# Kernel tuning notes

Measured on AMD Instinct MI355X. Metric: run time of the kernel, lower is better.

## Reference

```python
import jax, jax.numpy as jnp
import numpy as np

N = 4096          # batch of candidate observations
D = 1024          # embedding dim
N_CLASSES = 100
GTG_MAX_ITER = 30 # gtg_tol=0.0 -> while loop always runs max_iter steps
PERC_LABELED = 0.5
EPS = 1e-8        # matches the +1e-08 in sum_X_A_X


def setup_inputs() -> dict:
    key = jax.random.key(0)
    k1, k2 = jax.random.split(key)
    embedding = jax.random.normal(k1, (N, D), dtype=jnp.float32)
    labels = jax.random.randint(k2, (N,), 0, N_CLASSES, dtype=jnp.int32)
    return {"embedding": embedding, "labels": labels}


def _cos_affinity(E):
    # F.normalize(E, dim=-1) with eps=1e-12, then relu(En @ En.T), diag := 1
    En = E / jnp.maximum(jnp.linalg.norm(E, axis=-1, keepdims=True), 1e-12)
    A = jax.nn.relu(En @ En.T)                      # [N, N]
    n = A.shape[0]
    idx = jnp.arange(n)
    A = A.at[idx, idx].set(1.0)
    return A, En


def reference(embedding, labels):
    n = embedding.shape[0]

    # ---- get_A_rbfk (A_function='cos_sim', rbf_aff=True) ----
    A, En = _cos_affinity(embedding)
    # 7th neighbor by descending cosine similarity (column index 6)
    idx7 = jnp.argsort(-A, axis=1)[:, 6]            # [N]
    # sigma_i = relu(cos(x_i, seventh_i)) -- the [0,1] entry of the 2x2 cos-sim matrix
    sigmas = jax.nn.relu(jnp.sum(En * En[idx7], axis=-1))  # [N]
    A = jnp.exp(-(A ** 2) / (sigmas[:, None] * sigmas[None, :]))

    # ---- threshold (strategy='mean', cos_sim branch) ----
    A = jnp.where(A < jnp.mean(A), 0.0, A)

    # ---- get_X: first n_lab indices labeled (one-hot), rest uniform 1/C ----
    n_lab = int(n * PERC_LABELED)
    labeled = jnp.arange(n) < n_lab                 # [N] bool
    one_hot = jax.nn.one_hot(labels, N_CLASSES, dtype=jnp.float32)
    X0 = jnp.where(labeled[:, None], one_hot, jnp.float32(1.0 / N_CLASSES))

    # ---- graph transduction game: X <- (X + X*(A@X)) / rowsum ----
    def step(X, _):
        mm_A_X = A @ X                              # [N, C]
        mult = X + X * mm_A_X
        Xn = mult / (jnp.sum(mult, axis=1, keepdims=True) + EPS)
        ent = -jnp.sum(Xn * jnp.log(Xn + EPS), axis=1)  # per-row entropy history
        return Xn, ent

    Xf, _ent_hist = jax.lax.scan(step, X0, None, length=GTG_MAX_ITER)
    return Xf
```

## Files before the change

### kernel.cpp

```cpp
#include <hip/hip_runtime.h>
#include <math.h>

typedef unsigned short ushortT;
typedef __attribute__((ext_vector_type(8))) short short8;
typedef __attribute__((ext_vector_type(4))) float f32x4;

#define NN 4096
#define DD 1024
#define NC 100
#define CP 128
#define NLAB 2048
#define NITER 30

__device__ __forceinline__ ushortT bf16rn(float x) {
  unsigned u = __float_as_uint(x);
  unsigned r = (u + 0x7fffu + ((u >> 16) & 1u)) >> 16;
  return (ushortT)r;
}
__device__ __forceinline__ float bf2f(ushortT h) {
  return __uint_as_float(((unsigned)h) << 16);
}
__device__ __forceinline__ void gload16(const void* g, void* l) {
  __builtin_amdgcn_global_load_lds((const __attribute__((address_space(1))) char*)g,
                                   (__attribute__((address_space(3))) char*)l, 16, 0, 0);
}

__global__ __launch_bounds__(256) void k_normalize(const float* __restrict__ E,
                                                   ushortT* __restrict__ Enh) {
  int row = blockIdx.x, t = threadIdx.x;
  const float4* e4 = (const float4*)(E + (size_t)row * DD);
  float4 v = e4[t];
  float ss = v.x * v.x + v.y * v.y + v.z * v.z + v.w * v.w;
  __shared__ float red[4];
  int lane = t & 63, w = t >> 6;
#pragma unroll
  for (int off = 32; off; off >>= 1) ss += __shfl_xor(ss, off);
  if (lane == 0) red[w] = ss;
  __syncthreads();
  float tot = red[0] + red[1] + red[2] + red[3];
  float d = fmaxf(sqrtf(tot), 1e-12f);
  ushort4 hv;
  hv.x = bf16rn(v.x / d); hv.y = bf16rn(v.y / d);
  hv.z = bf16rn(v.z / d); hv.w = bf16rn(v.w / d);
  ((ushort4*)Enh)[(size_t)row * 256 + t] = hv;
}

__global__ __launch_bounds__(256, 4) void k_syrk_mfma(const ushortT* __restrict__ Enh,
                                                      ushortT* __restrict__ A) {
  int xg = (int)blockIdx.x & 7;
  int j = (int)blockIdx.x >> 3;
  int bi = -1, bj = 0;
#pragma unroll
  for (int p = 0; p < 4; ++p) {
    int bic = xg + (p << 3);
    int c = 32 - bic;
    if (bi < 0) {
      if (j < c) { bi = bic; bj = bic + j; } else j -= c;
    }
  }
  if (bi < 0) return;
  __shared__ ushortT lds[18432];
  int t = threadIdx.x;
  int l = t & 63, w = t >> 6;
  int i0 = bi << 7, j0 = bj << 7;
  int wr = w >> 1, wc = w & 1;
  f32x4 zz = {0.f, 0.f, 0.f, 0.f};
  f32x4 acc[4][4];
#pragma unroll
  for (int m = 0; m < 4; ++m)
#pragma unroll
    for (int n = 0; n < 4; ++n) acc[m][n] = zz;
  int arow_l = l & 15, kslot = l >> 4;

  for (int s = 0; s < 16; ++s) {
    int kk0 = s << 6;
#pragma unroll
    for (int q = 0; q < 4; ++q) {
      int n = (q << 8) + t;
      int r = n >> 3, p = n & 7;
      int col = (p ^ (r & 7)) << 3;
      gload16(Enh + (size_t)(i0 + r) * DD + kk0 + col, &lds[n << 3]);
      gload16(Enh + (size_t)(j0 + r) * DD + kk0 + col, &lds[8192 + (n << 3)]);
    }
    __syncthreads();
#pragma unroll
    for (int kk = 0; kk < 2; ++kk) {
      int g = (kk << 2) + kslot;
      short8 av[4], bv[4];
#pragma unroll
      for (int m = 0; m < 4; ++m) {
        int r = (wr << 6) + (m << 4) + arow_l;
        av[m] = *(const short8*)&lds[(r << 6) + ((g ^ (r & 7)) << 3)];
      }
#pragma unroll
      for (int n = 0; n < 4; ++n) {
        int r = (wc << 6) + (n << 4) + arow_l;
        bv[n] = *(const short8*)&lds[8192 + (r << 6) + ((g ^ (r & 7)) << 3)];
      }
#pragma unroll
      for (int m = 0; m < 4; ++m)
#pragma unroll
        for (int n = 0; n < 4; ++n)
          acc[m][n] = __builtin_amdgcn_mfma_f32_16x16x32_bf16(av[m], bv[n], acc[m][n], 0, 0, 0);
    }
    __syncthreads();
  }
  int rbase = (l >> 4) << 2;
#pragma unroll
  for (int m = 0; m < 4; ++m) {
#pragma unroll
    for (int n = 0; n < 4; ++n) {
#pragma unroll
      for (int r = 0; r < 4; ++r) {
        int gi = i0 + (wr << 6) + (m << 4) + rbase + r;
        int gj = j0 + (wc << 6) + (n << 4) + (l & 15);
        float v = fmaxf(acc[m][n][r], 0.0f);
        if (gi == gj) v = 1.0f;
        A[(size_t)gi * NN + gj] = bf16rn(v);
      }
    }
  }
  if (bi != bj) {
    float* T = (float*)&lds[0];
#pragma unroll
    for (int c2 = 0; c2 < 2; ++c2) {
      __syncthreads();
      if (wr == c2) {
#pragma unroll
        for (int m = 0; m < 4; ++m)
#pragma unroll
          for (int n = 0; n < 4; ++n)
#pragma unroll
            for (int r = 0; r < 4; ++r)
              T[(((wc << 6) + (n << 4) + (l & 15)) * 68) + (m << 4) + rbase + r] =
                  fmaxf(acc[m][n][r], 0.0f);
      }
      __syncthreads();
      int lj = t >> 1, cg = (t & 1) << 5;
#pragma unroll
      for (int q = 0; q < 4; ++q) {
        float4 a0 = *(const float4*)&T[lj * 68 + cg + (q << 3)];
        float4 a1 = *(const float4*)&T[lj * 68 + cg + (q << 3) + 4];
        short8 o;
        o[0] = (short)bf16rn(a0.x); o[1] = (short)bf16rn(a0.y);
        o[2] = (short)bf16rn(a0.z); o[3] = (short)bf16rn(a0.w);
        o[4] = (short)bf16rn(a1.x); o[5] = (short)bf16rn(a1.y);
        o[6] = (short)bf16rn(a1.z); o[7] = (short)bf16rn(a1.w);
        *(short8*)&A[(size_t)(j0 + lj) * NN + i0 + (c2 << 6) + cg + (q << 3)] = o;
      }
    }
  }
}

__device__ __forceinline__ void ins7(float (&tv)[7], float v) {
  if (v > tv[6]) {
#pragma unroll
    for (int s = 0; s < 7; s++) {
      if (v > tv[s]) { float tmp = tv[s]; tv[s] = v; v = tmp; }
    }
  }
}
__global__ __launch_bounds__(256) void k_top7(const ushortT* __restrict__ A,
                                              float* __restrict__ sig) {
  int w = threadIdx.x >> 6, lane = threadIdx.x & 63;
  int row = (blockIdx.x << 2) + w;
  const ushortT* a = A + (size_t)row * NN;
  float tv[7];
#pragma unroll
  for (int i = 0; i < 7; i++) tv[i] = -1.0f;
#pragma unroll
  for (int k = 0; k < 8; k++) {
    short8 v = *(const short8*)(a + (k << 9) + (lane << 3));
#pragma unroll
    for (int jj = 0; jj < 8; jj++) ins7(tv, bf2f((ushortT)v[jj]));
  }
  int head = 0;
  float seventh = 0.0f;
  for (int r = 0; r < 7; r++) {
    float h = (head < 7) ? tv[head] : -1.0f;
    float m = h;
#pragma unroll
    for (int off = 32; off; off >>= 1) m = fmaxf(m, __shfl_xor(m, off));
    unsigned long long ball = __ballot(h == m);
    if (lane == (__ffsll(ball) - 1)) head++;
    seventh = m;
  }
  if (lane == 0) sig[row] = seventh;
}

__global__ __launch_bounds__(256) void k_transform(const ushortT* __restrict__ A,
                                                   const float* __restrict__ sig,
                                                   double* __restrict__ parts) {
  int row = blockIdx.x;
  float si = sig[row];
  const ushortT* a = A + (size_t)row * NN;
  int t = threadIdx.x;
  double local = 0.0;
#pragma unroll
  for (int k = 0; k < 2; k++) {
    int idx = (k << 11) + (t << 3);
    short8 v = *(const short8*)(a + idx);
#pragma unroll
    for (int q = 0; q < 2; ++q) {
      float4 sg = *(const float4*)&sig[idx + (q << 2)];
      float s0 = bf2f((ushortT)v[(q << 2) + 0]);
      float s1 = bf2f((ushortT)v[(q << 2) + 1]);
      float s2 = bf2f((ushortT)v[(q << 2) + 2]);
      float s3 = bf2f((ushortT)v[(q << 2) + 3]);
      local += (double)expf(-(s0 * s0) / (si * sg.x)) +
               (double)expf(-(s1 * s1) / (si * sg.y)) +
               (double)expf(-(s2 * s2) / (si * sg.z)) +
               (double)expf(-(s3 * s3) / (si * sg.w));
    }
  }
  __shared__ double dred[4];
  int lane = t & 63, wv = t >> 6;
#pragma unroll
  for (int off = 32; off; off >>= 1) local += __shfl_xor(local, off);
  if (lane == 0) dred[wv] = local;
  __syncthreads();
  if (t == 0) parts[row] = dred[0] + dred[1] + dred[2] + dred[3];
}

__global__ __launch_bounds__(256) void k_mean(const double* __restrict__ parts,
                                              float* __restrict__ meanb) {
  int t = threadIdx.x;
  double local = 0.0;
#pragma unroll
  for (int k = 0; k < NN / 256; k++) local += parts[(k << 8) + t];
  __shared__ double dred[4];
  int lane = t & 63, wv = t >> 6;
#pragma unroll
  for (int off = 32; off; off >>= 1) local += __shfl_xor(local, off);
  if (lane == 0) dred[wv] = local;
  __syncthreads();
  if (t == 0) meanb[0] = (float)((dred[0] + dred[1] + dred[2] + dred[3]) / ((double)NN * (double)NN));
}

__global__ __launch_bounds__(256) void k_thresh_pack(const ushortT* __restrict__ A,
                                                     const float* __restrict__ sig,
                                                     const float* __restrict__ meanb,
                                                     ushortT* __restrict__ ApL,
                                                     ushortT* __restrict__ ApU) {
  float m = meanb[0];
  int i8 = ((int)blockIdx.x << 8) + threadIdx.x;
  int row2 = i8 >> 9;
  int col8 = (i8 & 511) << 3;
  int grow = NLAB + row2;
  float si = sig[grow];
  short8 v = *(const short8*)&A[(size_t)grow * NN + col8];
  short8 o;
#pragma unroll
  for (int q = 0; q < 2; ++q) {
    float4 sg = *(const float4*)&sig[col8 + (q << 2)];
    float s0 = bf2f((ushortT)v[(q << 2) + 0]);
    float s1 = bf2f((ushortT)v[(q << 2) + 1]);
    float s2 = bf2f((ushortT)v[(q << 2) + 2]);
    float s3 = bf2f((ushortT)v[(q << 2) + 3]);
    float c0 = expf(-(s0 * s0) / (si * sg.x));
    float c1 = expf(-(s1 * s1) / (si * sg.y));
    float c2 = expf(-(s2 * s2) / (si * sg.z));
    float c3 = expf(-(s3 * s3) / (si * sg.w));
    o[(q << 2) + 0] = (short)((c0 < m) ? 0 : bf16rn(c0));
    o[(q << 2) + 1] = (short)((c1 < m) ? 0 : bf16rn(c1));
    o[(q << 2) + 2] = (short)((c2 < m) ? 0 : bf16rn(c2));
    o[(q << 2) + 3] = (short)((c3 < m) ? 0 : bf16rn(c3));
  }
  int half = col8 >> 11;
  int cc = col8 & 2047;
  int rt = row2 >> 4, arow = row2 & 15;
  int kc = cc >> 5, khi = (cc >> 3) & 3;
  ushortT* dst = half ? ApU : ApL;
  *(short8*)&dst[((size_t)((rt << 6) + kc) << 9) + (khi << 7) + (arow << 3)] = o;
}

__global__ __launch_bounds__(256) void k_xlabp(const int* __restrict__ labels,
                                               ushortT* __restrict__ Xlabp) {
  int idx = ((int)blockIdx.x << 8) + threadIdx.x;
  int c = idx >> 11, j = idx & 2047;
  int kc = j >> 5, khi = (j >> 3) & 3, k0 = j & 7;
  int cf = c >> 4, slot = c & 15;
  Xlabp[((size_t)(((kc << 3) + cf) << 2) + khi) * 128 + (slot << 3) + k0] =
      (labels[j] == c) ? (ushortT)0x3F80 : (ushortT)0;
}

__global__ __launch_bounds__(64) void k_xinit(float* __restrict__ Xf,
                                              ushortT* __restrict__ Xp) {
  int rt = blockIdx.x, l = threadIdx.x;
  int col = l & 15, rg4 = l >> 4;
  int kc = rt >> 1;
  int kk = ((rt & 1) << 4) + (rg4 << 2);
  int khi = kk >> 3, k0 = kk & 7;
#pragma unroll
  for (int cf = 0; cf < 8; ++cf) {
    int cls = (cf << 4) + col;
    float v = (cls < NC) ? 0.01f : 0.0f;
    ((f32x4*)Xf)[(size_t)((rt << 3) + cf) * 64 + l] = (f32x4){v, v, v, v};
    ushortT h = bf16rn(v);
    ushort4 hv = {h, h, h, h};
    *(ushort4*)&Xp[((size_t)(((kc << 3) + cf) << 2) + khi) * 128 + (col << 3) + k0] = hv;
  }
}

__global__ __launch_bounds__(256) void k_gP(const ushortT* __restrict__ Ap,
                                            const ushortT* __restrict__ Xp,
                                            float* __restrict__ Pp) {
  int t = threadIdx.x, l = t & 63, w = t >> 6;
  int bid = (int)blockIdx.x;
  int rt = ((bid & 7) << 4) + ((bid >> 3) & 15);
  int s = bid >> 7;
  int kc0 = (s << 4) + (w << 2);
  const ushortT* ab = Ap + ((size_t)rt << 15) + ((size_t)kc0 << 9) + (l << 3);
  const ushortT* xb = Xp + ((size_t)kc0 << 12) + (l << 3);
  short8 av[4];
#pragma unroll
  for (int i = 0; i < 4; ++i) av[i] = *(const short8*)(ab + ((size_t)i << 9));
  f32x4 acc[8];
#pragma unroll
  for (int cf = 0; cf < 8; ++cf) {
    acc[cf] = (f32x4){0.f, 0.f, 0.f, 0.f};
#pragma unroll
    for (int i = 0; i < 4; ++i) {
      short8 bv = *(const short8*)(xb + ((size_t)i << 12) + (cf << 9));
      acc[cf] = __builtin_amdgcn_mfma_f32_16x16x32_bf16(av[i], bv, acc[cf], 0, 0, 0);
    }
  }
  __shared__ float red[4][8][64][4];
#pragma unroll
  for (int cf = 0; cf < 8; ++cf) *(f32x4*)&red[w][cf][l][0] = acc[cf];
  __syncthreads();
  if (w < 2) {
#pragma unroll
    for (int q = 0; q < 4; ++q) {
      int cf = (w << 2) + q;
      f32x4 sum = *(const f32x4*)&red[0][cf][l][0];
#pragma unroll
      for (int wp = 1; wp < 4; ++wp) {
        f32x4 p = *(const f32x4*)&red[wp][cf][l][0];
        sum[0] += p[0]; sum[1] += p[1]; sum[2] += p[2]; sum[3] += p[3];
      }
      ((f32x4*)Pp)[((size_t)(((s << 7) + rt) << 3) + cf) * 64 + l] = sum;
    }
  }
}

__global__ __launch_bounds__(64) void k_updY(const float* __restrict__ Pp,
                                             float* __restrict__ YlabF) {
  int rt = blockIdx.x, l = threadIdx.x;
#pragma unroll
  for (int cf = 0; cf < 8; ++cf) {
    f32x4 acc = (f32x4){0.f, 0.f, 0.f, 0.f};
#pragma unroll
    for (int s = 0; s < 4; ++s) {
      f32x4 p = ((const f32x4*)Pp)[((size_t)(((s << 7) + rt) << 3) + cf) * 64 + l];
      acc[0] += p[0]; acc[1] += p[1]; acc[2] += p[2]; acc[3] += p[3];
    }
    ((f32x4*)YlabF)[(size_t)((rt << 3) + cf) * 64 + l] = acc;
  }
}

__global__ __launch_bounds__(256) void k_it2(
    const ushortT* __restrict__ Ap, const ushortT* __restrict__ Xp,
    const float* __restrict__ YlabF, const float* __restrict__ XfPrev,
    float* __restrict__ XfOut, ushortT* __restrict__ XpOut,
    float* __restrict__ sums2, int* __restrict__ cnt2) {
  __shared__ float red[4][4][64][4];
  __shared__ float sums_l[4][16];
  __shared__ float totl[16];
  int t = threadIdx.x, l = t & 63, w = t >> 6;
  int bid = (int)blockIdx.x;
  int rt = ((bid & 7) << 4) + ((bid >> 3) & 15);
  int half = bid >> 7;
  int cf = (half << 2) + w;

  const ushortT* ab = Ap + ((size_t)rt << 15) + ((size_t)(w << 4) << 9) + (l << 3);
  const ushortT* xb = Xp + ((size_t)(w << 4) << 12) + ((size_t)(half << 2) << 9) + (l << 3);
  f32x4 acc[4];
#pragma unroll
  for (int cc = 0; cc < 4; ++cc) acc[cc] = (f32x4){0.f, 0.f, 0.f, 0.f};
#pragma unroll
  for (int i = 0; i < 16; ++i) {
    short8 av = *(const short8*)(ab + ((size_t)i << 9));
#pragma unroll
    for (int cc = 0; cc < 4; ++cc) {
      short8 bv = *(const short8*)(xb + ((size_t)i << 12) + (cc << 9));
      acc[cc] = __builtin_amdgcn_mfma_f32_16x16x32_bf16(av, bv, acc[cc], 0, 0, 0);
    }
  }
#pragma unroll
  for (int cc = 0; cc < 4; ++cc) *(f32x4*)&red[w][cc][l][0] = acc[cc];
  __syncthreads();
  f32x4 mm = (f32x4){0.f, 0.f, 0.f, 0.f};
#pragma unroll
  for (int wp = 0; wp < 4; ++wp) {
    f32x4 p = *(const f32x4*)&red[wp][w][l][0];
    mm[0] += p[0]; mm[1] += p[1]; mm[2] += p[2]; mm[3] += p[3];
  }
  size_t fo = (size_t)((rt << 3) + cf) * 64 + l;
  f32x4 yl = ((const f32x4*)YlabF)[fo];
  f32x4 xv = ((const f32x4*)XfPrev)[fo];
  f32x4 mult, rs;
#pragma unroll
  for (int r = 0; r < 4; ++r) {
    mult[r] = fmaf(xv[r], mm[r] + yl[r], xv[r]);
    rs[r] = mult[r];
  }
#pragma unroll
  for (int msk = 1; msk < 16; msk <<= 1) {
#pragma unroll
    for (int r = 0; r < 4; ++r) rs[r] += __shfl_xor(rs[r], msk);
  }
  int rg4 = l >> 4, col16 = l & 15;
  if (col16 == 0) {
#pragma unroll
    for (int r = 0; r < 4; ++r) sums_l[w][(rg4 << 2) + r] = rs[r];
  }
  __syncthreads();
  if (w == 0 && l < 16) {
    float hs = sums_l[0][l] + sums_l[1][l] + sums_l[2][l] + sums_l[3][l];
    atomicAdd(&sums2[(rt << 4) + l], hs);
  }
  if (t == 0) {
    asm volatile("s_waitcnt vmcnt(0)" ::: "memory");
    atomicAdd(&cnt2[rt], 1);
    while (atomicAdd(&cnt2[rt], 0) < 2) __builtin_amdgcn_s_sleep(2);
  }
  __syncthreads();
  if (w == 0 && l < 16) totl[l] = atomicAdd(&sums2[(rt << 4) + l], 0.0f) + 1e-8f;
  __syncthreads();
  f32x4 ov;
#pragma unroll
  for (int r = 0; r < 4; ++r) ov[r] = mult[r] / totl[(rg4 << 2) + r];
  ((f32x4*)XfOut)[fo] = ov;
  int kcp = rt >> 1;
  int rem = ((rt & 1) << 4) + (rg4 << 2);
  int khi = rem >> 3, k0 = rem & 7;
  ushort4 xo;
  xo.x = bf16rn(ov[0]); xo.y = bf16rn(ov[1]);
  xo.z = bf16rn(ov[2]); xo.w = bf16rn(ov[3]);
  *(ushort4*)&XpOut[((size_t)(((kcp << 3) + cf) << 2) + khi) * 128 + (col16 << 3) + k0] = xo;
}

__global__ __launch_bounds__(256) void k_output(const float* __restrict__ Xf,
                                                const int* __restrict__ labels,
                                                float* __restrict__ out) {
  int idx = ((int)blockIdx.x << 8) + threadIdx.x;
  int i = idx / NC, c = idx - i * NC;
  float v;
  if (i < NLAB) {
    v = (labels[i] == c) ? 1.0f : 0.0f;
  } else {
    int row = i - NLAB;
    int rt = row >> 4, r = row & 15;
    int rg4 = r >> 2, reg = r & 3;
    int cf = c >> 4, col = c & 15;
    v = Xf[((size_t)(((rt << 3) + cf) << 6) + (rg4 << 4) + col) * 4 + reg];
  }
  out[idx] = v;
}

extern "C" void kernel_launch(void* const* d_in, const int* in_sizes, int n_in,
                              void* d_out, int out_size, void* d_ws, size_t ws_size,
                              hipStream_t stream) {
  const float* E = (const float*)d_in[0];
  const int* labels = (const int*)d_in[1];
  float* out = (float*)d_out;
  char* ws = (char*)d_ws;
  const size_t MB = 1024 * 1024;

  ushortT* A = (ushortT*)ws;
  ushortT* Enh = (ushortT*)(ws + 32 * MB);
  ushortT* ApL = (ushortT*)(ws + 40 * MB);
  ushortT* ApU = (ushortT*)(ws + 48 * MB);
  float* sig = (float*)(ws + 56 * MB);
  double* parts = (double*)(ws + 56 * MB + 65536);
  float* meanb = (float*)(ws + 56 * MB + 131072);
  ushortT* Xlabp = (ushortT*)(ws + 57 * MB);
  float* YlabF = (float*)(ws + 58 * MB);
  float* Xf0 = (float*)(ws + 59 * MB);
  float* Xf1 = (float*)(ws + 60 * MB);
  ushortT* Xp0 = (ushortT*)(ws + 61 * MB);
  ushortT* Xp1 = (ushortT*)(ws + 62 * MB);
  float* Pp = (float*)(ws + 64 * MB);
  float* sums2 = (float*)(ws + 68 * MB);
  int* cnt2 = (int*)(ws + 69 * MB);

  k_normalize<<<NN, 256, 0, stream>>>(E, Enh);
  k_syrk_mfma<<<640, 256, 0, stream>>>(Enh, A);
  k_top7<<<NN / 4, 256, 0, stream>>>(A, sig);
  k_transform<<<NN, 256, 0, stream>>>(A, sig, parts);
  k_mean<<<1, 256, 0, stream>>>(parts, meanb);
  k_thresh_pack<<<4096, 256, 0, stream>>>(A, sig, meanb, ApL, ApU);
  k_xlabp<<<1024, 256, 0, stream>>>(labels, Xlabp);
  k_xinit<<<128, 64, 0, stream>>>(Xf0, Xp0);
  hipMemsetAsync(sums2, 0, (size_t)NITER * 128 * 16 * sizeof(float), stream);
  hipMemsetAsync(cnt2, 0, (size_t)NITER * 128 * sizeof(int), stream);
  k_gP<<<512, 256, 0, stream>>>(ApL, Xlabp, Pp);
  k_updY<<<128, 64, 0, stream>>>(Pp, YlabF);
  float* xf[2] = {Xf0, Xf1};
  ushortT* xp[2] = {Xp0, Xp1};
  int cur = 0;
  for (int it = 0; it < NITER; ++it) {
    int nxt = cur ^ 1;
    k_it2<<<256, 256, 0, stream>>>(ApU, xp[cur], YlabF, xf[cur], xf[nxt], xp[nxt],
                                   sums2 + (size_t)it * 2048, cnt2 + (size_t)it * 128);
    cur = nxt;
  }
  k_output<<<1600, 256, 0, stream>>>(xf[cur], labels, out);
}
```

Before: 428.8 us.

## Fuse GTG iterations into one persistent kernel with hierarchical grid barrier

Replaces the 30 per-iteration k_it2 launches plus the k_gP/k_updY precompute with a single persistent 256-block kernel. It computes the labeled-part product in-kernel, keeps X in registers, writes each iteration's bf16 X into its own buffer, and synchronises all blocks with a two-level atomic grid barrier. The aim is to remove kernel launch gaps and the global round-trips of Xf and YlabF. In exchange it relies on all 256 blocks being co-resident and on relaxed atomics giving correct visibility across blocks.

```diff
diff --git a/kernel.cpp b/kernel.cpp
--- a/kernel.cpp
+++ b/kernel.cpp
@@ -8,9 +8,9 @@
 #define NN 4096
 #define DD 1024
 #define NC 100
-#define CP 128
 #define NLAB 2048
 #define NITER 30
+#define XPBUF 262144
 
 __device__ __forceinline__ ushortT bf16rn(float x) {
   unsigned u = __float_as_uint(x);
@@ -284,8 +284,7 @@
       (labels[j] == c) ? (ushortT)0x3F80 : (ushortT)0;
 }
 
-__global__ __launch_bounds__(64) void k_xinit(float* __restrict__ Xf,
-                                              ushortT* __restrict__ Xp) {
+__global__ __launch_bounds__(64) void k_xinit(ushortT* __restrict__ Xp) {
   int rt = blockIdx.x, l = threadIdx.x;
   int col = l & 15, rg4 = l >> 4;
   int kc = rt >> 1;
@@ -295,75 +294,17 @@
   for (int cf = 0; cf < 8; ++cf) {
     int cls = (cf << 4) + col;
     float v = (cls < NC) ? 0.01f : 0.0f;
-    ((f32x4*)Xf)[(size_t)((rt << 3) + cf) * 64 + l] = (f32x4){v, v, v, v};
     ushortT h = bf16rn(v);
     ushort4 hv = {h, h, h, h};
     *(ushort4*)&Xp[((size_t)(((kc << 3) + cf) << 2) + khi) * 128 + (col << 3) + k0] = hv;
   }
 }
 
-__global__ __launch_bounds__(256) void k_gP(const ushortT* __restrict__ Ap,
-                                            const ushortT* __restrict__ Xp,
-                                            float* __restrict__ Pp) {
-  int t = threadIdx.x, l = t & 63, w = t >> 6;
-  int bid = (int)blockIdx.x;
-  int rt = ((bid & 7) << 4) + ((bid >> 3) & 15);
-  int s = bid >> 7;
-  int kc0 = (s << 4) + (w << 2);
-  const ushortT* ab = Ap + ((size_t)rt << 15) + ((size_t)kc0 << 9) + (l << 3);
-  const ushortT* xb = Xp + ((size_t)kc0 << 12) + (l << 3);
-  short8 av[4];
-#pragma unroll
-  for (int i = 0; i < 4; ++i) av[i] = *(const short8*)(ab + ((size_t)i << 9));
-  f32x4 acc[8];
-#pragma unroll
-  for (int cf = 0; cf < 8; ++cf) {
-    acc[cf] = (f32x4){0.f, 0.f, 0.f, 0.f};
-#pragma unroll
-    for (int i = 0; i < 4; ++i) {
-      short8 bv = *(const short8*)(xb + ((size_t)i << 12) + (cf << 9));
-      acc[cf] = __builtin_amdgcn_mfma_f32_16x16x32_bf16(av[i], bv, acc[cf], 0, 0, 0);
-    }
-  }
-  __shared__ float red[4][8][64][4];
-#pragma unroll
-  for (int cf = 0; cf < 8; ++cf) *(f32x4*)&red[w][cf][l][0] = acc[cf];
-  __syncthreads();
-  if (w < 2) {
-#pragma unroll
-    for (int q = 0; q < 4; ++q) {
-      int cf = (w << 2) + q;
-      f32x4 sum = *(const f32x4*)&red[0][cf][l][0];
-#pragma unroll
-      for (int wp = 1; wp < 4; ++wp) {
-        f32x4 p = *(const f32x4*)&red[wp][cf][l][0];
-        sum[0] += p[0]; sum[1] += p[1]; sum[2] += p[2]; sum[3] += p[3];
-      }
-      ((f32x4*)Pp)[((size_t)(((s << 7) + rt) << 3) + cf) * 64 + l] = sum;
-    }
-  }
-}
-
-__global__ __launch_bounds__(64) void k_updY(const float* __restrict__ Pp,
-                                             float* __restrict__ YlabF) {
-  int rt = blockIdx.x, l = threadIdx.x;
-#pragma unroll
-  for (int cf = 0; cf < 8; ++cf) {
-    f32x4 acc = (f32x4){0.f, 0.f, 0.f, 0.f};
-#pragma unroll
-    for (int s = 0; s < 4; ++s) {
-      f32x4 p = ((const f32x4*)Pp)[((size_t)(((s << 7) + rt) << 3) + cf) * 64 + l];
-      acc[0] += p[0]; acc[1] += p[1]; acc[2] += p[2]; acc[3] += p[3];
-    }
-    ((f32x4*)YlabF)[(size_t)((rt << 3) + cf) * 64 + l] = acc;
-  }
-}
-
-__global__ __launch_bounds__(256) void k_it2(
-    const ushortT* __restrict__ Ap, const ushortT* __restrict__ Xp,
-    const float* __restrict__ YlabF, const float* __restrict__ XfPrev,
-    float* __restrict__ XfOut, ushortT* __restrict__ XpOut,
-    float* __restrict__ sums2, int* __restrict__ cnt2) {
+__global__ __launch_bounds__(256) void k_persist(
+    const ushortT* __restrict__ ApL, const ushortT* __restrict__ ApU,
+    const ushortT* __restrict__ Xlabp, ushortT* __restrict__ XpBase,
+    float* __restrict__ Xf, float* __restrict__ sums2, int* __restrict__ cnt2,
+    int* __restrict__ gbar) {
   __shared__ float red[4][4][64][4];
   __shared__ float sums_l[4][16];
   __shared__ float totl[16];
@@ -372,73 +313,122 @@
   int rt = ((bid & 7) << 4) + ((bid >> 3) & 15);
   int half = bid >> 7;
   int cf = (half << 2) + w;
-
-  const ushortT* ab = Ap + ((size_t)rt << 15) + ((size_t)(w << 4) << 9) + (l << 3);
-  const ushortT* xb = Xp + ((size_t)(w << 4) << 12) + ((size_t)(half << 2) << 9) + (l << 3);
-  f32x4 acc[4];
-#pragma unroll
-  for (int cc = 0; cc < 4; ++cc) acc[cc] = (f32x4){0.f, 0.f, 0.f, 0.f};
-#pragma unroll
-  for (int i = 0; i < 16; ++i) {
-    short8 av = *(const short8*)(ab + ((size_t)i << 9));
-#pragma unroll
-    for (int cc = 0; cc < 4; ++cc) {
-      short8 bv = *(const short8*)(xb + ((size_t)i << 12) + (cc << 9));
-      acc[cc] = __builtin_amdgcn_mfma_f32_16x16x32_bf16(av, bv, acc[cc], 0, 0, 0);
-    }
-  }
-#pragma unroll
-  for (int cc = 0; cc < 4; ++cc) *(f32x4*)&red[w][cc][l][0] = acc[cc];
-  __syncthreads();
-  f32x4 mm = (f32x4){0.f, 0.f, 0.f, 0.f};
-#pragma unroll
-  for (int wp = 0; wp < 4; ++wp) {
-    f32x4 p = *(const f32x4*)&red[wp][w][l][0];
-    mm[0] += p[0]; mm[1] += p[1]; mm[2] += p[2]; mm[3] += p[3];
+  int rg4 = l >> 4, col16 = l & 15;
+
+  auto gemm = [&](const ushortT* __restrict__ Ap, const ushortT* __restrict__ Xp) -> f32x4 {
+    __syncthreads();
+    const ushortT* ab = Ap + ((size_t)rt << 15) + ((size_t)(w << 4) << 9) + (l << 3);
+    const ushortT* xb = Xp + ((size_t)(w << 4) << 12) + ((size_t)(half << 2) << 9) + (l << 3);
+    f32x4 acc[4];
+#pragma unroll
+    for (int cc = 0; cc < 4; ++cc) acc[cc] = (f32x4){0.f, 0.f, 0.f, 0.f};
+#pragma unroll
+    for (int i = 0; i < 16; ++i) {
+      short8 av = *(const short8*)(ab + ((size_t)i << 9));
+#pragma unroll
+      for (int cc = 0; cc < 4; ++cc) {
+        short8 bv = *(const short8*)(xb + ((size_t)i << 12) + (cc << 9));
+        acc[cc] = __builtin_amdgcn_mfma_f32_16x16x32_bf16(av, bv, acc[cc], 0, 0, 0);
+      }
+    }
+#pragma unroll
+    for (int cc = 0; cc < 4; ++cc) *(f32x4*)&red[w][cc][l][0] = acc[cc];
+    __syncthreads();
+    f32x4 mm = (f32x4){0.f, 0.f, 0.f, 0.f};
+#pragma unroll
+    for (int wp = 0; wp < 4; ++wp) {
+      f32x4 p = *(const f32x4*)&red[wp][w][l][0];
+      mm[0] += p[0]; mm[1] += p[1]; mm[2] += p[2]; mm[3] += p[3];
+    }
+    return mm;
+  };
+
+  f32x4 yl = gemm(ApL, Xlabp);
+  f32x4 x;
+  {
+    float v = ((cf << 4) + col16 < NC) ? 0.01f : 0.0f;
+    x[0] = v; x[1] = v; x[2] = v; x[3] = v;
+  }
+
+  for (int it = 0; it < NITER; ++it) {
+    f32x4 mm = gemm(ApU, XpBase + (size_t)it * XPBUF);
+    f32x4 mult, rs;
+#pragma unroll
+    for (int r = 0; r < 4; ++r) {
+      mult[r] = fmaf(x[r], mm[r] + yl[r], x[r]);
+      rs[r] = mult[r];
+    }
+#pragma unroll
+    for (int msk = 1; msk < 16; msk <<= 1) {
+#pragma unroll
+      for (int r = 0; r < 4; ++r) rs[r] += __shfl_xor(rs[r], msk);
+    }
+    if (col16 == 0) {
+#pragma unroll
+      for (int r = 0; r < 4; ++r) sums_l[w][(rg4 << 2) + r] = rs[r];
+    }
+    __syncthreads();
+    float* s2 = sums2 + ((size_t)it << 11);
+    int* c2 = cnt2 + (it << 7);
+    if (w == 0 && l < 16) {
+      float hs = sums_l[0][l] + sums_l[1][l] + sums_l[2][l] + sums_l[3][l];
+      atomicAdd(&s2[(rt << 4) + l], hs);
+    }
+    if (t == 0) {
+      asm volatile("s_waitcnt vmcnt(0)" ::: "memory");
+      atomicAdd(&c2[rt], 1);
+      while (atomicAdd(&c2[rt], 0) < 2) __builtin_amdgcn_s_sleep(1);
+    }
+    __syncthreads();
+    if (w == 0 && l < 16) totl[l] = atomicAdd(&s2[(rt << 4) + l], 0.0f) + 1e-8f;
+    __syncthreads();
+#pragma unroll
+    for (int r = 0; r < 4; ++r) x[r] = mult[r] / totl[(rg4 << 2) + r];
+
+    if (it < NITER - 1) {
+      ushortT* Xn = XpBase + (size_t)(it + 1) * XPBUF;
+      int kcp = rt >> 1;
+      int rem = ((rt & 1) << 4) + (rg4 << 2);
+      int khi = rem >> 3, k0 = rem & 7;
+      unsigned long long pk =
+          (unsigned long long)bf16rn(x[0]) |
+          ((unsigned long long)bf16rn(x[1]) << 16) |
+          ((unsigned long long)bf16rn(x[2]) << 32) |
+          ((unsigned long long)bf16rn(x[3]) << 48);
+      size_t off = ((size_t)(((kcp << 3) + cf) << 2) + khi) * 128 + (col16 << 3) + k0;
+      __hip_atomic_exchange((unsigned long long*)&Xn[off], pk, __ATOMIC_RELAXED,
+                            __HIP_MEMORY_SCOPE_AGENT);
+      asm volatile("s_waitcnt vmcnt(0)" ::: "memory");
+      __syncthreads();
+      if (t == 0) {
+        int* ga = gbar + it * 17;
+        int grp = bid >> 5;
+        int a = __hip_atomic_fetch_add(&ga[grp], 1, __ATOMIC_RELAXED,
+                                       __HIP_MEMORY_SCOPE_AGENT);
+        if (a == 31) {
+          int g2 = __hip_atomic_fetch_add(&ga[8], 1, __ATOMIC_RELAXED,
+                                          __HIP_MEMORY_SCOPE_AGENT);
+          if (g2 == 7) {
+#pragma unroll
+            for (int q = 0; q < 8; ++q)
+              __hip_atomic_fetch_add(&ga[9 + q], 1, __ATOMIC_RELAXED,
+                                     __HIP_MEMORY_SCOPE_AGENT);
+          } else {
+            while (__hip_atomic_fetch_add(&ga[9 + grp], 0, __ATOMIC_RELAXED,
+                                          __HIP_MEMORY_SCOPE_AGENT) == 0)
+              __builtin_amdgcn_s_sleep(1);
+          }
+        } else {
+          while (__hip_atomic_fetch_add(&ga[9 + grp], 0, __ATOMIC_RELAXED,
+                                        __HIP_MEMORY_SCOPE_AGENT) == 0)
+            __builtin_amdgcn_s_sleep(1);
+        }
+      }
+      __syncthreads();
+    }
   }
   size_t fo = (size_t)((rt << 3) + cf) * 64 + l;
-  f32x4 yl = ((const f32x4*)YlabF)[fo];
-  f32x4 xv = ((const f32x4*)XfPrev)[fo];
-  f32x4 mult, rs;
-#pragma unroll
-  for (int r = 0; r < 4; ++r) {
-    mult[r] = fmaf(xv[r], mm[r] + yl[r], xv[r]);
-    rs[r] = mult[r];
-  }
-#pragma unroll
-  for (int msk = 1; msk < 16; msk <<= 1) {
-#pragma unroll
-    for (int r = 0; r < 4; ++r) rs[r] += __shfl_xor(rs[r], msk);
-  }
-  int rg4 = l >> 4, col16 = l & 15;
-  if (col16 == 0) {
-#pragma unroll
-    for (int r = 0; r < 4; ++r) sums_l[w][(rg4 << 2) + r] = rs[r];
-  }
-  __syncthreads();
-  if (w == 0 && l < 16) {
-    float hs = sums_l[0][l] + sums_l[1][l] + sums_l[2][l] + sums_l[3][l];
-    atomicAdd(&sums2[(rt << 4) + l], hs);
-  }
-  if (t == 0) {
-    asm volatile("s_waitcnt vmcnt(0)" ::: "memory");
-    atomicAdd(&cnt2[rt], 1);
-    while (atomicAdd(&cnt2[rt], 0) < 2) __builtin_amdgcn_s_sleep(2);
-  }
-  __syncthreads();
-  if (w == 0 && l < 16) totl[l] = atomicAdd(&sums2[(rt << 4) + l], 0.0f) + 1e-8f;
-  __syncthreads();
-  f32x4 ov;
-#pragma unroll
-  for (int r = 0; r < 4; ++r) ov[r] = mult[r] / totl[(rg4 << 2) + r];
-  ((f32x4*)XfOut)[fo] = ov;
-  int kcp = rt >> 1;
-  int rem = ((rt & 1) << 4) + (rg4 << 2);
-  int khi = rem >> 3, k0 = rem & 7;
-  ushort4 xo;
-  xo.x = bf16rn(ov[0]); xo.y = bf16rn(ov[1]);
-  xo.z = bf16rn(ov[2]); xo.w = bf16rn(ov[3]);
-  *(ushort4*)&XpOut[((size_t)(((kcp << 3) + cf) << 2) + khi) * 128 + (col16 << 3) + k0] = xo;
+  ((f32x4*)Xf)[fo] = x;
 }
 
 __global__ __launch_bounds__(256) void k_output(const float* __restrict__ Xf,
@@ -476,14 +466,11 @@
   double* parts = (double*)(ws + 56 * MB + 65536);
   float* meanb = (float*)(ws + 56 * MB + 131072);
   ushortT* Xlabp = (ushortT*)(ws + 57 * MB);
-  float* YlabF = (float*)(ws + 58 * MB);
-  float* Xf0 = (float*)(ws + 59 * MB);
-  float* Xf1 = (float*)(ws + 60 * MB);
-  ushortT* Xp0 = (ushortT*)(ws + 61 * MB);
-  ushortT* Xp1 = (ushortT*)(ws + 62 * MB);
-  float* Pp = (float*)(ws + 64 * MB);
-  float* sums2 = (float*)(ws + 68 * MB);
-  int* cnt2 = (int*)(ws + 69 * MB);
+  float* Xf = (float*)(ws + 58 * MB);
+  ushortT* XpBase = (ushortT*)(ws + 64 * MB);
+  float* sums2 = (float*)(ws + 80 * MB);
+  int* cnt2 = (int*)(ws + 81 * MB);
+  int* gbar = (int*)(ws + 82 * MB);
 
   k_normalize<<<NN, 256, 0, stream>>>(E, Enh);
   k_syrk_mfma<<<640, 256, 0, stream>>>(Enh, A);
@@ -492,19 +479,10 @@
   k_mean<<<1, 256, 0, stream>>>(parts, meanb);
   k_thresh_pack<<<4096, 256, 0, stream>>>(A, sig, meanb, ApL, ApU);
   k_xlabp<<<1024, 256, 0, stream>>>(labels, Xlabp);
-  k_xinit<<<128, 64, 0, stream>>>(Xf0, Xp0);
-  hipMemsetAsync(sums2, 0, (size_t)NITER * 128 * 16 * sizeof(float), stream);
+  k_xinit<<<128, 64, 0, stream>>>(XpBase);
+  hipMemsetAsync(sums2, 0, (size_t)NITER * 2048 * sizeof(float), stream);
   hipMemsetAsync(cnt2, 0, (size_t)NITER * 128 * sizeof(int), stream);
-  k_gP<<<512, 256, 0, stream>>>(ApL, Xlabp, Pp);
-  k_updY<<<128, 64, 0, stream>>>(Pp, YlabF);
-  float* xf[2] = {Xf0, Xf1};
-  ushortT* xp[2] = {Xp0, Xp1};
-  int cur = 0;
-  for (int it = 0; it < NITER; ++it) {
-    int nxt = cur ^ 1;
-    k_it2<<<256, 256, 0, stream>>>(ApU, xp[cur], YlabF, xf[cur], xf[nxt], xp[nxt],
-                                   sums2 + (size_t)it * 2048, cnt2 + (size_t)it * 128);
-    cur = nxt;
-  }
-  k_output<<<1600, 256, 0, stream>>>(xf[cur], labels, out);
-}
+  hipMemsetAsync(gbar, 0, (size_t)NITER * 17 * sizeof(int), stream);
+  k_persist<<<256, 256, 0, stream>>>(ApL, ApU, Xlabp, XpBase, Xf, sums2, cnt2, gbar);
+  k_output<<<1600, 256, 0, stream>>>(Xf, labels, out);
+}
```

After: 499.1 us. 1.16x slower.

## Split GTG iteration kernel across four column-quarter blocks per row-tile pair

Applied to the files above, without the earlier changes.

The per-iteration A@X kernel is regridded. Each 512-thread block now handles two row tiles and one quarter of the class columns, with 8 waves splitting the K dimension, instead of one row tile and half the columns with 4 waves. Row sums are exchanged through per-quarter slots in global memory, and a spin barrier waits for 8 arrivals per row-tile pair. The aim is to halve the per-wave MFMA chain and widen the parallelism. In exchange the cross-block reduction and synchronisation involve more blocks, and half the waves sit idle during the epilogue.

```diff
diff --git a/kernel.cpp b/kernel.cpp
--- a/kernel.cpp
+++ b/kernel.cpp
@@ -8,7 +8,6 @@
 #define NN 4096
 #define DD 1024
 #define NC 100
-#define CP 128
 #define NLAB 2048
 #define NITER 30
 
@@ -359,86 +358,107 @@
   }
 }
 
-__global__ __launch_bounds__(256) void k_it2(
+__global__ __launch_bounds__(512) void k_it3(
     const ushortT* __restrict__ Ap, const ushortT* __restrict__ Xp,
     const float* __restrict__ YlabF, const float* __restrict__ XfPrev,
     float* __restrict__ XfOut, ushortT* __restrict__ XpOut,
-    float* __restrict__ sums2, int* __restrict__ cnt2) {
-  __shared__ float red[4][4][64][4];
-  __shared__ float sums_l[4][16];
-  __shared__ float totl[16];
+    float* __restrict__ sums4, int* __restrict__ cnt4) {
+  __shared__ float red[8][2][64][4];
+  __shared__ float sums_l[2][2][16];
+  __shared__ float totl[2][16];
   int t = threadIdx.x, l = t & 63, w = t >> 6;
   int bid = (int)blockIdx.x;
-  int rt = ((bid & 7) << 4) + ((bid >> 3) & 15);
-  int half = bid >> 7;
-  int cf = (half << 2) + w;
-
-  const ushortT* ab = Ap + ((size_t)rt << 15) + ((size_t)(w << 4) << 9) + (l << 3);
-  const ushortT* xb = Xp + ((size_t)(w << 4) << 12) + ((size_t)(half << 2) << 9) + (l << 3);
-  f32x4 acc[4];
-#pragma unroll
-  for (int cc = 0; cc < 4; ++cc) acc[cc] = (f32x4){0.f, 0.f, 0.f, 0.f};
+  int rtp = ((bid & 7) << 3) + ((bid >> 3) & 7);
+  int q = bid >> 6;
+  int h = w >> 2, kq = w & 3;
+  int rt = (rtp << 1) + h;
+  int kc0 = kq << 4;
+  int rg4 = l >> 4, col16 = l & 15;
+
+  const ushortT* ab = Ap + ((size_t)rt << 15) + ((size_t)kc0 << 9) + (l << 3);
+  const ushortT* xb = Xp + ((size_t)kc0 << 12) + ((size_t)(q << 1) << 9) + (l << 3);
+  f32x4 acc[2];
+  acc[0] = (f32x4){0.f, 0.f, 0.f, 0.f};
+  acc[1] = (f32x4){0.f, 0.f, 0.f, 0.f};
 #pragma unroll
   for (int i = 0; i < 16; ++i) {
     short8 av = *(const short8*)(ab + ((size_t)i << 9));
 #pragma unroll
-    for (int cc = 0; cc < 4; ++cc) {
+    for (int cc = 0; cc < 2; ++cc) {
       short8 bv = *(const short8*)(xb + ((size_t)i << 12) + (cc << 9));
       acc[cc] = __builtin_amdgcn_mfma_f32_16x16x32_bf16(av, bv, acc[cc], 0, 0, 0);
     }
   }
-#pragma unroll
-  for (int cc = 0; cc < 4; ++cc) *(f32x4*)&red[w][cc][l][0] = acc[cc];
-  __syncthreads();
+  *(f32x4*)&red[w][0][l][0] = acc[0];
+  *(f32x4*)&red[w][1][l][0] = acc[1];
+  __syncthreads();
+
+  bool owner = ((w & 3) < 2);
+  int cc = w & 3;
+  int cf = (q << 1) + cc;
   f32x4 mm = (f32x4){0.f, 0.f, 0.f, 0.f};
-#pragma unroll
-  for (int wp = 0; wp < 4; ++wp) {
-    f32x4 p = *(const f32x4*)&red[wp][w][l][0];
-    mm[0] += p[0]; mm[1] += p[1]; mm[2] += p[2]; mm[3] += p[3];
-  }
-  size_t fo = (size_t)((rt << 3) + cf) * 64 + l;
-  f32x4 yl = ((const f32x4*)YlabF)[fo];
-  f32x4 xv = ((const f32x4*)XfPrev)[fo];
-  f32x4 mult, rs;
-#pragma unroll
-  for (int r = 0; r < 4; ++r) {
-    mult[r] = fmaf(xv[r], mm[r] + yl[r], xv[r]);
-    rs[r] = mult[r];
-  }
-#pragma unroll
-  for (int msk = 1; msk < 16; msk <<= 1) {
-#pragma unroll
-    for (int r = 0; r < 4; ++r) rs[r] += __shfl_xor(rs[r], msk);
-  }
-  int rg4 = l >> 4, col16 = l & 15;
-  if (col16 == 0) {
-#pragma unroll
-    for (int r = 0; r < 4; ++r) sums_l[w][(rg4 << 2) + r] = rs[r];
-  }
-  __syncthreads();
-  if (w == 0 && l < 16) {
-    float hs = sums_l[0][l] + sums_l[1][l] + sums_l[2][l] + sums_l[3][l];
-    atomicAdd(&sums2[(rt << 4) + l], hs);
+  f32x4 mult = mm;
+  if (owner) {
+#pragma unroll
+    for (int k = 0; k < 4; ++k) {
+      f32x4 p = *(const f32x4*)&red[(h << 2) + k][cc][l][0];
+      mm[0] += p[0]; mm[1] += p[1]; mm[2] += p[2]; mm[3] += p[3];
+    }
+    size_t fo = (size_t)((rt << 3) + cf) * 64 + l;
+    f32x4 yl = ((const f32x4*)YlabF)[fo];
+    f32x4 xv = ((const f32x4*)XfPrev)[fo];
+    f32x4 rs;
+#pragma unroll
+    for (int r = 0; r < 4; ++r) {
+      mult[r] = fmaf(xv[r], mm[r] + yl[r], xv[r]);
+      rs[r] = mult[r];
+    }
+#pragma unroll
+    for (int msk = 1; msk < 16; msk <<= 1) {
+#pragma unroll
+      for (int r = 0; r < 4; ++r) rs[r] += __shfl_xor(rs[r], msk);
+    }
+    if (col16 == 0) {
+#pragma unroll
+      for (int r = 0; r < 4; ++r) sums_l[h][cc][(rg4 << 2) + r] = rs[r];
+    }
+  }
+  __syncthreads();
+  if ((w == 0 || w == 4) && l < 16) {
+    float bp = sums_l[h][0][l] + sums_l[h][1][l];
+    __hip_atomic_exchange(&sums4[((size_t)rt << 6) + (q << 4) + l], bp,
+                          __ATOMIC_RELAXED, __HIP_MEMORY_SCOPE_AGENT);
+  }
+  if ((w == 0 || w == 4) && l == 0) {
+    asm volatile("s_waitcnt vmcnt(0)" ::: "memory");
+    atomicAdd(&cnt4[rtp], 1);
   }
   if (t == 0) {
-    asm volatile("s_waitcnt vmcnt(0)" ::: "memory");
-    atomicAdd(&cnt2[rt], 1);
-    while (atomicAdd(&cnt2[rt], 0) < 2) __builtin_amdgcn_s_sleep(2);
-  }
-  __syncthreads();
-  if (w == 0 && l < 16) totl[l] = atomicAdd(&sums2[(rt << 4) + l], 0.0f) + 1e-8f;
-  __syncthreads();
-  f32x4 ov;
-#pragma unroll
-  for (int r = 0; r < 4; ++r) ov[r] = mult[r] / totl[(rg4 << 2) + r];
-  ((f32x4*)XfOut)[fo] = ov;
-  int kcp = rt >> 1;
-  int rem = ((rt & 1) << 4) + (rg4 << 2);
-  int khi = rem >> 3, k0 = rem & 7;
-  ushort4 xo;
-  xo.x = bf16rn(ov[0]); xo.y = bf16rn(ov[1]);
-  xo.z = bf16rn(ov[2]); xo.w = bf16rn(ov[3]);
-  *(ushort4*)&XpOut[((size_t)(((kcp << 3) + cf) << 2) + khi) * 128 + (col16 << 3) + k0] = xo;
+    while (atomicAdd(&cnt4[rtp], 0) < 8) __builtin_amdgcn_s_sleep(1);
+  }
+  __syncthreads();
+  if ((w == 0 || w == 4) && l < 16) {
+    float s = 1e-8f;
+#pragma unroll
+    for (int qq = 0; qq < 4; ++qq)
+      s += atomicAdd(&sums4[((size_t)rt << 6) + (qq << 4) + l], 0.0f);
+    totl[h][l] = s;
+  }
+  __syncthreads();
+  if (owner) {
+    f32x4 ov;
+#pragma unroll
+    for (int r = 0; r < 4; ++r) ov[r] = mult[r] / totl[h][(rg4 << 2) + r];
+    size_t fo = (size_t)((rt << 3) + cf) * 64 + l;
+    ((f32x4*)XfOut)[fo] = ov;
+    int kcp = rt >> 1;
+    int rem = ((rt & 1) << 4) + (rg4 << 2);
+    int khi = rem >> 3, k0 = rem & 7;
+    ushort4 xo;
+    xo.x = bf16rn(ov[0]); xo.y = bf16rn(ov[1]);
+    xo.z = bf16rn(ov[2]); xo.w = bf16rn(ov[3]);
+    *(ushort4*)&XpOut[((size_t)(((kcp << 3) + cf) << 2) + khi) * 128 + (col16 << 3) + k0] = xo;
+  }
 }
 
 __global__ __launch_bounds__(256) void k_output(const float* __restrict__ Xf,
@@ -482,8 +502,8 @@
   ushortT* Xp0 = (ushortT*)(ws + 61 * MB);
   ushortT* Xp1 = (ushortT*)(ws + 62 * MB);
   float* Pp = (float*)(ws + 64 * MB);
-  float* sums2 = (float*)(ws + 68 * MB);
-  int* cnt2 = (int*)(ws + 69 * MB);
+  float* sums4 = (float*)(ws + 68 * MB);
+  int* cnt4 = (int*)(ws + 69 * MB);
 
   k_normalize<<<NN, 256, 0, stream>>>(E, Enh);
   k_syrk_mfma<<<640, 256, 0, stream>>>(Enh, A);
@@ -493,8 +513,8 @@
   k_thresh_pack<<<4096, 256, 0, stream>>>(A, sig, meanb, ApL, ApU);
   k_xlabp<<<1024, 256, 0, stream>>>(labels, Xlabp);
   k_xinit<<<128, 64, 0, stream>>>(Xf0, Xp0);
-  hipMemsetAsync(sums2, 0, (size_t)NITER * 128 * 16 * sizeof(float), stream);
-  hipMemsetAsync(cnt2, 0, (size_t)NITER * 128 * sizeof(int), stream);
+  hipMemsetAsync(sums4, 0, (size_t)NITER * 128 * 4 * 16 * sizeof(float), stream);
+  hipMemsetAsync(cnt4, 0, (size_t)NITER * 64 * sizeof(int), stream);
   k_gP<<<512, 256, 0, stream>>>(ApL, Xlabp, Pp);
   k_updY<<<128, 64, 0, stream>>>(Pp, YlabF);
   float* xf[2] = {Xf0, Xf1};
@@ -502,8 +522,8 @@
   int cur = 0;
   for (int it = 0; it < NITER; ++it) {
     int nxt = cur ^ 1;
-    k_it2<<<256, 256, 0, stream>>>(ApU, xp[cur], YlabF, xf[cur], xf[nxt], xp[nxt],
-                                   sums2 + (size_t)it * 2048, cnt2 + (size_t)it * 128);
+    k_it3<<<256, 512, 0, stream>>>(ApU, xp[cur], YlabF, xf[cur], xf[nxt], xp[nxt],
+                                   sums4 + (size_t)it * 8192, cnt4 + (size_t)it * 64);
     cur = nxt;
   }
   k_output<<<1600, 256, 0, stream>>>(xf[cur], labels, out);
```

Result: no change. 421.6 us (-1.7%).
